# Kernel tuning notes

Measured on AMD Instinct MI355X. Metric: run time of the kernel, lower is better.

## Reference

```python
import jax, jax.numpy as jnp
import numpy as np

N_USERS = 50000
N_ITEMS = 100000
N_ENT = 200000
N_REL_TOTAL = 32  # n_relations * 2
DIM = 64
N_INTENTS = 2
N_LAYERS = 1
B = 4096
E_KG = 2_000_000
E_UI_HALF = 1_000_000  # user->item interactions; symmetrized to 2M directed edges


def setup_inputs() -> dict:
    key = jax.random.key(0)
    ks = jax.random.split(key, 16)
    s = 0.05  # xavier-ish scale
    user_emb = jax.random.normal(ks[0], (N_USERS, DIM), jnp.float32) * s
    entity_emb = jax.random.normal(ks[1], (N_ENT, DIM), jnp.float32) * s
    relation_emb = jax.random.normal(ks[2], (N_REL_TOTAL, DIM), jnp.float32) * s
    intent_weights = jax.random.normal(ks[3], (N_INTENTS, N_REL_TOTAL), jnp.float32) * s
    router_w = jax.random.normal(ks[4], (N_INTENTS, DIM), jnp.float32) * s
    router_b = jnp.zeros((N_INTENTS,), jnp.float32)
    kg_w = jax.random.normal(ks[5], (N_LAYERS, DIM, DIM), jnp.float32) * (1.0 / np.sqrt(DIM))
    item2entity = jax.random.randint(ks[6], (N_ITEMS,), 0, N_ENT)
    kg_src = jax.random.randint(ks[7], (E_KG,), 0, N_ENT)
    kg_dst = jax.random.randint(ks[8], (E_KG,), 0, N_ENT)
    kg_rel = jax.random.randint(ks[9], (E_KG,), 0, N_REL_TOTAL)
    # UI bipartite graph, symmetrically normalized (D^-1/2 A D^-1/2), as in _build_ui_graph
    rng = np.random.default_rng(0)
    uu = rng.integers(0, N_USERS, E_UI_HALF)
    ii = rng.integers(0, N_ITEMS, E_UI_HALF) + N_USERS
    rows = np.concatenate([uu, ii])
    cols = np.concatenate([ii, uu])
    n_nodes = N_USERS + N_ITEMS
    deg = np.bincount(rows, minlength=n_nodes).astype(np.float32)
    dinv = np.where(deg > 0, deg ** -0.5, 0.0).astype(np.float32)
    ui_vals = jnp.asarray(dinv[rows] * dinv[cols])
    ui_row = jnp.asarray(rows.astype(np.int32))
    ui_col = jnpseq = jnp.asarray(cols.astype(np.int32))
    u = jax.random.randint(ks[10], (B,), 0, N_USERS)
    i = jax.random.randint(ks[11], (B,), 0, N_ITEMS)
    neg_i = jax.random.randint(ks[12], (B,), 0, N_ITEMS)
    return dict(u=u, i=i, neg_i=neg_i,
                user_emb=user_emb, entity_emb=entity_emb, relation_emb=relation_emb,
                intent_weights=intent_weights, router_w=router_w, router_b=router_b,
                kg_w=kg_w, ui_vals=ui_vals,
                item2entity=item2entity, kg_src=kg_src, kg_dst=kg_dst, kg_rel=kg_rel,
                ui_row=ui_row, ui_col=ui_col)


def _l2norm(x):
    return x / jnp.maximum(jnp.linalg.norm(x, axis=-1, keepdims=True), 1e-12)


def reference(u, i, neg_i, user_emb, entity_emb, relation_emb, intent_weights,
              router_w, router_b, kg_w, ui_vals, item2entity, kg_src, kg_dst,
              kg_rel, ui_row, ui_col):
    n_ent = entity_emb.shape[0]
    # ---- _propagate_kg (dropout in eval mode = identity) ----
    x = entity_emb
    gate = jax.nn.sigmoid(relation_emb[kg_rel])  # [E, D]
    deg = jax.ops.segment_sum(jnp.ones(kg_dst.shape[0], jnp.float32), kg_dst,
                              num_segments=n_ent)
    deg = jnp.maximum(deg, 1.0)[:, None]
    for l in range(kg_w.shape[0]):
        msg = (x[kg_src] @ kg_w[l].T) * gate           # gather + linear + gate
        agg = jax.ops.segment_sum(msg, kg_dst, num_segments=n_ent)
        x = _l2norm(jax.nn.elu(agg / deg + x))
    item_kg = x[item2entity]                            # [n_items, D]
    # ---- _propagate_ui: sparse normalized adj propagation ----
    all_emb = jnp.concatenate([user_emb, item_kg], 0)
    n_nodes = all_emb.shape[0]
    embs = [all_emb]
    for _ in range(N_LAYERS):
        all_emb = jax.ops.segment_sum(ui_vals[:, None] * all_emb[ui_col], ui_row,
                                      num_segments=n_nodes)
        embs.append(all_emb)
    final = jnp.mean(jnp.stack(embs, 1), 1)
    n_users = user_emb.shape[0]
    u_prop, i_prop = final[:n_users], final[n_users:]
    # ---- intent mixing ----
    intent_dist = jax.nn.softmax(u_prop @ router_w.T + router_b, axis=-1)
    intent_emb = jax.nn.softmax(intent_weights, axis=-1) @ relation_emb
    ue = u_prop + intent_dist @ intent_emb
    ie = i_prop + item_kg
    pos = jnp.sum(ue[u] * ie[i], 1)
    neg = jnp.sum(ue[u] * ie[neg_i], 1)
    return pos, neg
```

## Files before the change

kernel.cpp:

```cpp
#include <hip/hip_runtime.h>
#include <math.h>

#define N_USERS 50000
#define N_ITEMS 100000
#define N_ENT   200000
#define N_NODES (N_USERS + N_ITEMS)
#define N_REL   32
#define DIM     64

#define NB_KG  391
#define NB_UI  586
#define NB_TOT (NB_KG + NB_UI)
#define CAPK   4096
#define CAPU   1536
#define NMMTILE 1563
#define NSCAT  768
#define FUSE_GRID (NSCAT + NMMTILE)
#define NCPY   208

__device__ __forceinline__ unsigned short f2bf(float f) {
    unsigned u = __float_as_uint(f);
    u += 0x7FFFu + ((u >> 16) & 1u);
    return (unsigned short)(u >> 16);
}
__device__ __forceinline__ float bf_lo(unsigned v) { return __uint_as_float(v << 16); }
__device__ __forceinline__ float bf_hi(unsigned v) { return __uint_as_float(v & 0xFFFF0000u); }
__device__ __forceinline__ int getbit(const unsigned* m, int i) {
    return (m[i >> 5] >> (i & 31)) & 1;
}

__global__ __launch_bounds__(256) void build_masks(const int* __restrict__ i2e,
                                                   const int* __restrict__ u,
                                                   const int* __restrict__ ipos,
                                                   const int* __restrict__ ineg,
                                                   const float* __restrict__ rel_emb,
                                                   float2* __restrict__ gateg,
                                                   unsigned* __restrict__ ent_mask,
                                                   unsigned* __restrict__ node_mask,
                                                   int* __restrict__ bcur,
                                                   int B) {
    int t = blockIdx.x * 256 + threadIdx.x;
    int stride = gridDim.x * 256;
    for (int i = threadIdx.x; i < NB_TOT; i += 256)
        bcur[i] = (i < NB_KG) ? i * CAPK : (i - NB_KG) * CAPU;
    if (blockIdx.x == 0) {
        for (int idx = threadIdx.x; idx < N_REL * 32; idx += 256) {
            int rel = idx >> 5, hl2 = idx & 31;
            float g0 = 1.0f / (1.0f + __expf(-rel_emb[rel * 64 + 2 * hl2]));
            float g1 = 1.0f / (1.0f + __expf(-rel_emb[rel * 64 + 2 * hl2 + 1]));
            gateg[idx] = make_float2(g0, g1);
        }
    }
    for (int i = t; i < N_ITEMS; i += stride) {
        int e = i2e[i];
        atomicOr(&ent_mask[e >> 5], 1u << (e & 31));
    }
    for (int i = t; i < 3 * B; i += stride) {
        int r = (i < B) ? u[i]
              : (i < 2 * B) ? N_USERS + ipos[i - B]
                            : N_USERS + ineg[i - 2 * B];
        atomicOr(&node_mask[r >> 5], 1u << (r & 31));
    }
}

__global__ __launch_bounds__(512) void mm_scatter(const float* __restrict__ x,
                                                  const float* __restrict__ w,
                                                  unsigned short* __restrict__ y16,
                                                  int n_ent,
                                                  const int* __restrict__ kg_src,
                                                  const int* __restrict__ kg_dst,
                                                  const int* __restrict__ kg_rel,
                                                  const int* __restrict__ ui_row,
                                                  const int* __restrict__ ui_col,
                                                  const float* __restrict__ ui_vals,
                                                  const unsigned* __restrict__ ent_mask,
                                                  const unsigned* __restrict__ node_mask,
                                                  int* __restrict__ bcur,
                                                  unsigned int* __restrict__ kgrec,
                                                  int* __restrict__ uirec,
                                                  float* __restrict__ uval,
                                                  int e_kg, int e_ui) {
    __shared__ __align__(16) char smem[49152];
    int tid = threadIdx.x;
    int bid = blockIdx.x;

    if (bid < NSCAT) {
        int* h     = (int*)smem;
        int* lbase = h + NB_TOT;
        int n = e_kg + e_ui;
        int nchunks = (n + 4095) >> 12;
        for (int c = bid; c < nchunks; c += NSCAT) {
            int base = c << 12;
            for (int i = tid; i < NB_TOT; i += 512) h[i] = 0;
            __syncthreads();
            unsigned int rec[8];
            float val[8];
            int bk[8];
            #pragma unroll
            for (int j = 0; j < 8; j++) {
                int e = base + j * 512 + tid;
                bk[j] = -1;
                if (e < n) {
                    if (e < e_kg) {
                        int d = kg_dst[e];
                        if (getbit(ent_mask, d)) {
                            bk[j]  = d >> 9;
                            rec[j] = (unsigned int)kg_src[e]
                                     | ((unsigned int)kg_rel[e] << 18)
                                     | ((unsigned int)(d & 511) << 23);
                            atomicAdd(&h[bk[j]], 1);
                        }
                    } else {
                        int i2 = e - e_kg;
                        int r  = ui_row[i2];
                        if (getbit(node_mask, r)) {
                            bk[j]  = NB_KG + (r >> 8);
                            rec[j] = (unsigned int)ui_col[i2]
                                     | ((unsigned int)(r & 255) << 18);
                            val[j] = ui_vals[i2];
                            atomicAdd(&h[bk[j]], 1);
                        }
                    }
                }
            }
            __syncthreads();
            for (int i = tid; i < NB_TOT; i += 512) {
                int cc = h[i];
                lbase[i] = cc ? atomicAdd(&bcur[i], cc) : 0;
            }
            __syncthreads();
            #pragma unroll
            for (int j = 0; j < 8; j++) {
                if (bk[j] >= 0) {
                    int pos = atomicAdd(&lbase[bk[j]], 1);
                    if (bk[j] < NB_KG) {
                        if (pos < (bk[j] + 1) * CAPK) kgrec[pos] = rec[j];
                    } else {
                        int bu = bk[j] - NB_KG;
                        if (pos < (bu + 1) * CAPU) { uirec[pos] = (int)rec[j]; uval[pos] = val[j]; }
                    }
                }
            }
            __syncthreads();
        }
        return;
    }

    int mtile = bid - NSCAT;
    float (*xt)[128] = (float (*)[128])smem;
    float (*wt)[64]  = (float (*)[64])(smem + 32768);
    int base = mtile * 128;

    #pragma unroll
    for (int q = 0; q < 2; q++) {
        int idx = q * 512 + tid;
        int j = idx >> 4, k4 = idx & 15;
        int s0 = (k4 << 2) & 28;
        float4 v = ((const float4*)w)[idx];
        wt[4 * k4 + 0][j ^ s0] = v.x;
        wt[4 * k4 + 1][j ^ s0] = v.y;
        wt[4 * k4 + 2][j ^ s0] = v.z;
        wt[4 * k4 + 3][j ^ s0] = v.w;
    }
    #pragma unroll
    for (int q = 0; q < 4; q++) {
        int idx = q * 512 + tid;
        int r = idx >> 4, k4 = idx & 15;
        int gr = base + r;
        int s0 = (k4 << 2) & 28;
        if (gr < n_ent) {
            float4 v = ((const float4*)x)[(long)gr * 16 + k4];
            xt[4 * k4 + 0][r ^ s0] = v.x;
            xt[4 * k4 + 1][r ^ s0] = v.y;
            xt[4 * k4 + 2][r ^ s0] = v.z;
            xt[4 * k4 + 3][r ^ s0] = v.w;
        }
    }
    __syncthreads();

    int j0 = (tid & 7) * 8;
    int r0 = (tid >> 3) * 2;
    float acc[2][8];
    #pragma unroll
    for (int i = 0; i < 2; i++)
        #pragma unroll
        for (int j = 0; j < 8; j++) acc[i][j] = 0.f;

    #pragma unroll 4
    for (int k = 0; k < 64; k++) {
        int s = k & 28;
        float2 xa = *(const float2*)&xt[k][r0 ^ s];
        float4 wa = *(const float4*)&wt[k][j0 ^ s];
        float4 wb = *(const float4*)&wt[k][(j0 + 4) ^ s];
        float xr[2] = {xa.x, xa.y};
        float wr[8] = {wa.x, wa.y, wa.z, wa.w, wb.x, wb.y, wb.z, wb.w};
        #pragma unroll
        for (int i = 0; i < 2; i++)
            #pragma unroll
            for (int j = 0; j < 8; j++)
                acc[i][j] += xr[i] * wr[j];
    }

    #pragma unroll
    for (int i = 0; i < 2; i++) {
        int gr = base + r0 + i;
        if (gr < n_ent) {
            uint4 o;
            o.x = (unsigned)f2bf(acc[i][0]) | ((unsigned)f2bf(acc[i][1]) << 16);
            o.y = (unsigned)f2bf(acc[i][2]) | ((unsigned)f2bf(acc[i][3]) << 16);
            o.z = (unsigned)f2bf(acc[i][4]) | ((unsigned)f2bf(acc[i][5]) << 16);
            o.w = (unsigned)f2bf(acc[i][6]) | ((unsigned)f2bf(acc[i][7]) << 16);
            *(uint4*)&y16[(long)gr * 64 + j0] = o;
        }
    }
}

__global__ __launch_bounds__(256) void bucket_finalize(const int* __restrict__ bcur,
                                                       unsigned int* __restrict__ kgrec,
                                                       int* __restrict__ uirec,
                                                       float* __restrict__ uval,
                                                       int* __restrict__ beg_kg,
                                                       int* __restrict__ end_kg,
                                                       int* __restrict__ beg_ui,
                                                       int* __restrict__ end_ui,
                                                       const float* __restrict__ user_emb,
                                                       unsigned short* __restrict__ all16) {
    __shared__ unsigned int rec[CAPK];
    __shared__ float fval[CAPU];
    __shared__ int hist[512];
    int tid = threadIdx.x;

    if (blockIdx.x >= NB_TOT) {
        int cid = blockIdx.x - NB_TOT;
        const float4* ue4 = (const float4*)user_emb;
        uint2* a2 = (uint2*)all16;
        int total = N_USERS * 16;
        for (int i = cid * 256 + tid; i < total; i += NCPY * 256) {
            float4 v = ue4[i];
            a2[i] = make_uint2((unsigned)f2bf(v.x) | ((unsigned)f2bf(v.y) << 16),
                               (unsigned)f2bf(v.z) | ((unsigned)f2bf(v.w) << 16));
        }
        return;
    }

    bool iskg = blockIdx.x < NB_KG;
    int  b    = iskg ? blockIdx.x : blockIdx.x - NB_KG;
    int base  = iskg ? b * CAPK : b * CAPU;
    int cap   = iskg ? CAPK : CAPU;
    int ne    = min(bcur[blockIdx.x] - base, cap);
    int key_base = iskg ? (b << 9) : (b << 8);
    int nkeys = iskg ? min(512, N_ENT - key_base) : min(256, N_NODES - key_base);
    int SH = iskg ? 23 : 18;

    for (int i = tid; i < ne; i += 256) {
        if (iskg) rec[i] = kgrec[base + i];
        else { rec[i] = (unsigned int)uirec[base + i]; fval[i] = uval[base + i]; }
    }
    for (int i = tid; i < 512; i += 256) hist[i] = 0;
    __syncthreads();
    for (int i = tid; i < ne; i += 256)
        atomicAdd(&hist[rec[i] >> SH], 1);
    __syncthreads();
    int i0 = tid, i1 = tid + 256;
    int v0 = hist[i0], v1 = hist[i1];
    __syncthreads();
    for (int o = 1; o < 512; o <<= 1) {
        int a0 = (i0 >= o) ? hist[i0 - o] : 0;
        int a1 = (i1 >= o) ? hist[i1 - o] : 0;
        __syncthreads();
        hist[i0] += a0; hist[i1] += a1;
        __syncthreads();
    }
    int e0 = hist[i0] - v0, e1 = hist[i1] - v1;
    __syncthreads();
    hist[i0] = e0; hist[i1] = e1;
    int* begg = iskg ? beg_kg : beg_ui;
    int* endg = iskg ? end_kg : end_ui;
    if (i0 < nkeys) { begg[key_base + i0] = base + e0; endg[key_base + i0] = base + e0 + v0; }
    if (i1 < nkeys) { begg[key_base + i1] = base + e1; endg[key_base + i1] = base + e1 + v1; }
    __syncthreads();
    for (int i = tid; i < ne; i += 256) {
        unsigned int r = rec[i];
        int k = r >> SH;
        int slot = atomicAdd(&hist[k], 1);
        if (iskg) kgrec[base + slot] = r & 0x7FFFFFu;
        else      { uirec[base + slot] = (int)(r & 0x3FFFFu); uval[base + slot] = fval[i]; }
    }
}

__global__ __launch_bounds__(256) void kgagg_build(const int* __restrict__ beg_kg,
                                                   const int* __restrict__ end_kg,
                                                   const unsigned int* __restrict__ packed,
                                                   const unsigned short* __restrict__ y16,
                                                   const float* __restrict__ entity_emb,
                                                   const int* __restrict__ i2e,
                                                   const float4* __restrict__ gate4,
                                                   const unsigned* __restrict__ node_mask,
                                                   float* __restrict__ all_emb,
                                                   unsigned short* __restrict__ all16) {
    int lane = threadIdx.x & 63;
    int half = lane >> 5;
    int hl   = lane & 31;
    int duo  = hl >> 4;
    int ql   = hl & 15;
    long wpair = (long)((blockIdx.x * 256 + threadIdx.x) >> 6);
    int it = (int)(wpair * 2 + half);
    if (it >= N_ITEMS) return;
    int w = N_USERS + it;

    int ent = i2e[it];
    const uint2* y2 = (const uint2*)y16;
    int beg = beg_kg[ent], end = end_kg[ent];
    float a0 = 0.f, a1 = 0.f, a2 = 0.f, a3 = 0.f;
    float b0 = 0.f, b1 = 0.f, b2 = 0.f, b3 = 0.f;
    int p = beg;
    for (; p + 4 <= end; p += 4) {
        unsigned pk0 = packed[p + duo];
        unsigned pk1 = packed[p + 2 + duo];
        uint2 v0 = y2[(long)(pk0 & 0x3FFFF) * 16 + ql];
        uint2 v1 = y2[(long)(pk1 & 0x3FFFF) * 16 + ql];
        float4 g0 = gate4[(pk0 >> 18) * 16 + ql];
        float4 g1 = gate4[(pk1 >> 18) * 16 + ql];
        a0 += bf_lo(v0.x) * g0.x;  a1 += bf_hi(v0.x) * g0.y;
        a2 += bf_lo(v0.y) * g0.z;  a3 += bf_hi(v0.y) * g0.w;
        b0 += bf_lo(v1.x) * g1.x;  b1 += bf_hi(v1.x) * g1.y;
        b2 += bf_lo(v1.y) * g1.z;  b3 += bf_hi(v1.y) * g1.w;
    }
    if (p + duo < end) {
        unsigned pk = packed[p + duo];
        uint2 v = y2[(long)(pk & 0x3FFFF) * 16 + ql];
        float4 g = gate4[(pk >> 18) * 16 + ql];
        a0 += bf_lo(v.x) * g.x;  a1 += bf_hi(v.x) * g.y;
        a2 += bf_lo(v.y) * g.z;  a3 += bf_hi(v.y) * g.w;
    }
    if (p + 2 + duo < end) {
        unsigned pk = packed[p + 2 + duo];
        uint2 v = y2[(long)(pk & 0x3FFFF) * 16 + ql];
        float4 g = gate4[(pk >> 18) * 16 + ql];
        b0 += bf_lo(v.x) * g.x;  b1 += bf_hi(v.x) * g.y;
        b2 += bf_lo(v.y) * g.z;  b3 += bf_hi(v.y) * g.w;
    }
    a0 += b0; a1 += b1; a2 += b2; a3 += b3;
    a0 += __shfl_xor(a0, 16);
    a1 += __shfl_xor(a1, 16);
    a2 += __shfl_xor(a2, 16);
    a3 += __shfl_xor(a3, 16);

    float deg = fmaxf((float)(end - beg), 1.0f);
    float4 xv = ((const float4*)entity_emb)[(long)ent * 16 + ql];
    float v0 = a0 / deg + xv.x;
    float v1 = a1 / deg + xv.y;
    float v2 = a2 / deg + xv.z;
    float v3 = a3 / deg + xv.w;
    v0 = (v0 > 0.0f) ? v0 : (__expf(v0) - 1.0f);
    v1 = (v1 > 0.0f) ? v1 : (__expf(v1) - 1.0f);
    v2 = (v2 > 0.0f) ? v2 : (__expf(v2) - 1.0f);
    v3 = (v3 > 0.0f) ? v3 : (__expf(v3) - 1.0f);
    float ss = v0 * v0 + v1 * v1 + v2 * v2 + v3 * v3;
    ss += __shfl_xor(ss, 1);
    ss += __shfl_xor(ss, 2);
    ss += __shfl_xor(ss, 4);
    ss += __shfl_xor(ss, 8);
    float inv = 1.0f / fmaxf(sqrtf(ss), 1e-12f);
    if (duo == 0) {
        float r0 = v0 * inv, r1 = v1 * inv, r2 = v2 * inv, r3 = v3 * inv;
        if (getbit(node_mask, w))
            ((float4*)all_emb)[(long)w * 16 + ql] = make_float4(r0, r1, r2, r3);
        ((uint2*)all16)[(long)w * 16 + ql] =
            make_uint2((unsigned)f2bf(r0) | ((unsigned)f2bf(r1) << 16),
                       (unsigned)f2bf(r2) | ((unsigned)f2bf(r3) << 16));
    }
}

__global__ __launch_bounds__(256) void ui_aggregate_s(const int* __restrict__ beg_ui,
                                                      const int* __restrict__ end_ui,
                                                      const int* __restrict__ colrec,
                                                      const float* __restrict__ uval,
                                                      const float* __restrict__ all_emb,
                                                      const float* __restrict__ user_emb,
                                                      const unsigned short* __restrict__ all16,
                                                      const int* __restrict__ u,
                                                      const int* __restrict__ ipos,
                                                      const int* __restrict__ ineg,
                                                      float* __restrict__ final_emb, int B) {
    const uint2* a2p = (const uint2*)all16;
    int lane = threadIdx.x & 63;
    int half = lane >> 5;
    int hl   = lane & 31;
    int duo  = hl >> 4;
    int ql   = hl & 15;
    long wpair = (long)((blockIdx.x * 256 + threadIdx.x) >> 6);
    int s = (int)(wpair * 2 + half);
    if (s >= 3 * B) return;
    int r;
    if (s < B)          r = u[s];
    else if (s < 2 * B) r = N_USERS + ipos[s - B];
    else                r = N_USERS + ineg[s - 2 * B];

    int beg = beg_ui[r], end = end_ui[r];
    float a0 = 0.f, a1 = 0.f, a2 = 0.f, a3 = 0.f;
    float b0 = 0.f, b1 = 0.f, b2 = 0.f, b3 = 0.f;
    int p = beg;
    for (; p + 4 <= end; p += 4) {
        int   c0 = colrec[p + duo];
        int   c1 = colrec[p + 2 + duo];
        float d0 = uval[p + duo];
        float d1 = uval[p + 2 + duo];
        uint2 v0 = a2p[(long)c0 * 16 + ql];
        uint2 v1 = a2p[(long)c1 * 16 + ql];
        a0 += d0 * bf_lo(v0.x);  a1 += d0 * bf_hi(v0.x);
        a2 += d0 * bf_lo(v0.y);  a3 += d0 * bf_hi(v0.y);
        b0 += d1 * bf_lo(v1.x);  b1 += d1 * bf_hi(v1.x);
        b2 += d1 * bf_lo(v1.y);  b3 += d1 * bf_hi(v1.y);
    }
    if (p + duo < end) {
        int   c = colrec[p + duo];
        float d = uval[p + duo];
        uint2 v = a2p[(long)c * 16 + ql];
        a0 += d * bf_lo(v.x);  a1 += d * bf_hi(v.x);
        a2 += d * bf_lo(v.y);  a3 += d * bf_hi(v.y);
    }
    if (p + 2 + duo < end) {
        int   c = colrec[p + 2 + duo];
        float d = uval[p + 2 + duo];
        uint2 v = a2p[(long)c * 16 + ql];
        b0 += d * bf_lo(v.x);  b1 += d * bf_hi(v.x);
        b2 += d * bf_lo(v.y);  b3 += d * bf_hi(v.y);
    }
    a0 += b0; a1 += b1; a2 += b2; a3 += b3;
    a0 += __shfl_xor(a0, 16);
    a1 += __shfl_xor(a1, 16);
    a2 += __shfl_xor(a2, 16);
    a3 += __shfl_xor(a3, 16);
    if (duo == 0) {
        float4 ae = (r < N_USERS)
            ? ((const float4*)user_emb)[(long)r * 16 + ql]
            : ((const float4*)all_emb)[(long)r * 16 + ql];
        ((float4*)final_emb)[(long)r * 16 + ql] =
            make_float4(0.5f * (ae.x + a0), 0.5f * (ae.y + a1),
                        0.5f * (ae.z + a2), 0.5f * (ae.w + a3));
    }
}

__global__ void final_kernel(const int* __restrict__ u, const int* __restrict__ ipos,
                             const int* __restrict__ ineg,
                             const float* __restrict__ final_emb,
                             const float* __restrict__ all_emb,
                             const float* __restrict__ rw, const float* __restrict__ rb,
                             const float* __restrict__ iw, const float* __restrict__ rel_emb,
                             float* __restrict__ out, int B) {
    __shared__ float sh_intent[128];
    if (threadIdx.x < 64) {
        int j = threadIdx.x;
        for (int k = 0; k < 2; k++) {
            float m = -1e30f;
            for (int r = 0; r < N_REL; r++) m = fmaxf(m, iw[k * N_REL + r]);
            float Z = 0.f, acc = 0.f;
            for (int r = 0; r < N_REL; r++) {
                float e = __expf(iw[k * N_REL + r] - m);
                Z += e;
                acc += e * rel_emb[r * 64 + j];
            }
            sh_intent[k * 64 + j] = acc / Z;
        }
    }
    __syncthreads();
    int lane = threadIdx.x & 63;
    int wave = (blockIdx.x * blockDim.x + threadIdx.x) >> 6;
    int nw   = (gridDim.x * blockDim.x) >> 6;
    for (int b = wave; b < B; b += nw) {
        int uu = u[b];
        float up = final_emb[(long)uu * 64 + lane];
        float l0 = up * rw[lane];
        float l1 = up * rw[64 + lane];
        #pragma unroll
        for (int o = 32; o; o >>= 1) {
            l0 += __shfl_xor(l0, o);
            l1 += __shfl_xor(l1, o);
        }
        l0 += rb[0]; l1 += rb[1];
        float m  = fmaxf(l0, l1);
        float e0 = __expf(l0 - m), e1 = __expf(l1 - m);
        float inv = 1.0f / (e0 + e1);
        float p0 = e0 * inv, p1 = e1 * inv;
        float ue = up + p0 * sh_intent[lane] + p1 * sh_intent[64 + lane];

        int it = ipos[b];
        long rr = (long)(N_USERS + it) * 64 + lane;
        float ie = final_emb[rr] + all_emb[rr];
        float dp = ue * ie;
        #pragma unroll
        for (int o = 32; o; o >>= 1) dp += __shfl_xor(dp, o);
        if (lane == 0) out[b] = dp;

        it = ineg[b];
        rr = (long)(N_USERS + it) * 64 + lane;
        ie = final_emb[rr] + all_emb[rr];
        dp = ue * ie;
        #pragma unroll
        for (int o = 32; o; o >>= 1) dp += __shfl_xor(dp, o);
        if (lane == 0) out[B + b] = dp;
    }
}

extern "C" void kernel_launch(void* const* d_in, const int* in_sizes, int n_in,
                              void* d_out, int out_size, void* d_ws, size_t ws_size,
                              hipStream_t stream) {
    const int*   u          = (const int*)  d_in[0];
    const int*   ipos       = (const int*)  d_in[1];
    const int*   ineg       = (const int*)  d_in[2];
    const float* user_emb   = (const float*)d_in[3];
    const float* entity_emb = (const float*)d_in[4];
    const float* rel_emb    = (const float*)d_in[5];
    const float* iw         = (const float*)d_in[6];
    const float* rw         = (const float*)d_in[7];
    const float* rb         = (const float*)d_in[8];
    const float* kgw        = (const float*)d_in[9];
    const float* ui_vals    = (const float*)d_in[10];
    const int*   i2e        = (const int*)  d_in[11];
    const int*   kg_src     = (const int*)  d_in[12];
    const int*   kg_dst     = (const int*)  d_in[13];
    const int*   kg_rel     = (const int*)  d_in[14];
    const int*   ui_row     = (const int*)  d_in[15];
    const int*   ui_col     = (const int*)  d_in[16];
    float*       out        = (float*)d_out;

    int B    = in_sizes[0];
    int e_kg = in_sizes[12];
    int e_ui = in_sizes[15];

    char* ws = (char*)d_ws;
    unsigned short* y16       = (unsigned short*)(ws + 0);
    float*          all_emb   = (float*)(ws + 25600000);
    unsigned short* all16     = (unsigned short*)(ws + 64000000);
    float*          final_emb = (float*)(ws + 83200000);
    unsigned int*   kgrec     = (unsigned int*)(ws + 121600000);
    int*            end_kg    = (int*)(ws + 128006144);
    int*            end_ui    = (int*)(ws + 128806144);
    int*            uirec     = (int*)(ws + 129600000);
    float*          uval      = (float*)(ws + 133600000);
    int*            beg_kg    = (int*)(ws + 137600000);
    int*            beg_ui    = (int*)(ws + 138400256);
    unsigned*       ent_mask  = (unsigned*)(ws + 139000512);
    unsigned*       node_mask = (unsigned*)(ws + 139025600);
    int*            bcur      = (int*)(ws + 139608704);
    float2*         gateg     = (float2*)(ws + 139612672);

    hipMemsetAsync(ent_mask, 0, 25088 + 18752, stream);
    build_masks<<<512, 256, 0, stream>>>(i2e, u, ipos, ineg, rel_emb, gateg,
                                         ent_mask, node_mask, bcur, B);
    mm_scatter <<<FUSE_GRID, 512, 0, stream>>>(
        entity_emb, kgw, y16, N_ENT,
        kg_src, kg_dst, kg_rel, ui_row, ui_col, ui_vals,
        ent_mask, node_mask, bcur, kgrec, uirec, uval, e_kg, e_ui);
    bucket_finalize<<<NB_TOT + NCPY, 256, 0, stream>>>(bcur, kgrec, uirec, uval,
                                                       beg_kg, end_kg, beg_ui, end_ui,
                                                       user_emb, all16);
    {
        int nwaves = N_ITEMS / 2;
        int nblk   = (nwaves * 64 + 255) / 256;
        kgagg_build<<<nblk, 256, 0, stream>>>(
            beg_kg, end_kg, kgrec, y16, entity_emb, i2e,
            (const float4*)gateg, node_mask, all_emb, all16);
    }
    {
        int nwaves = (3 * B + 1) / 2;
        int nblk   = (nwaves * 64 + 255) / 256;
        ui_aggregate_s<<<nblk, 256, 0, stream>>>(
            beg_ui, end_ui, uirec, uval, all_emb, user_emb, all16,
            u, ipos, ineg, final_emb, B);
    }
    final_kernel<<<256, 256, 0, stream>>>(u, ipos, ineg, final_emb, all_emb,
                                          rw, rb, iw, rel_emb, out, B);
}
```

Measured before the change: 280.3 us.

## Split bucket finalize; fuse UI finalize and user copy into KG aggregation

The combined bucket_finalize kernel is split. KG bucket sorting stays in its own small kernel, while the UI bucket sort and the user-embedding bf16 copy move into extra blocks of the KG aggregation kernel. The UI work does not depend on the KG sort, so it can overlap with KG aggregation instead of sitting in the earlier launch. The cost is larger shared memory per block in the fused kernel, which can lower occupancy for the aggregation blocks.

```diff
diff --git a/kernel.cpp b/kernel.cpp
--- a/kernel.cpp
+++ b/kernel.cpp
@@ -17,6 +17,7 @@
 #define NSCAT  768
 #define FUSE_GRID (NSCAT + NMMTILE)
 #define NCPY   208
+#define KGOFF  (NB_UI + NCPY)
 
 __device__ __forceinline__ unsigned short f2bf(float f) {
     unsigned u = __float_as_uint(f);
@@ -215,51 +216,24 @@
     }
 }
 
-__global__ __launch_bounds__(256) void bucket_finalize(const int* __restrict__ bcur,
-                                                       unsigned int* __restrict__ kgrec,
-                                                       int* __restrict__ uirec,
-                                                       float* __restrict__ uval,
-                                                       int* __restrict__ beg_kg,
-                                                       int* __restrict__ end_kg,
-                                                       int* __restrict__ beg_ui,
-                                                       int* __restrict__ end_ui,
-                                                       const float* __restrict__ user_emb,
-                                                       unsigned short* __restrict__ all16) {
+__global__ __launch_bounds__(256) void finalize_kg(const int* __restrict__ bcur,
+                                                   unsigned int* __restrict__ kgrec,
+                                                   int* __restrict__ beg_kg,
+                                                   int* __restrict__ end_kg) {
     __shared__ unsigned int rec[CAPK];
-    __shared__ float fval[CAPU];
     __shared__ int hist[512];
+    int b    = blockIdx.x;
+    int base = b * CAPK;
+    int ne   = min(bcur[b] - base, CAPK);
+    int key_base = b << 9;
+    int nkeys = min(512, N_ENT - key_base);
     int tid = threadIdx.x;
 
-    if (blockIdx.x >= NB_TOT) {
-        int cid = blockIdx.x - NB_TOT;
-        const float4* ue4 = (const float4*)user_emb;
-        uint2* a2 = (uint2*)all16;
-        int total = N_USERS * 16;
-        for (int i = cid * 256 + tid; i < total; i += NCPY * 256) {
-            float4 v = ue4[i];
-            a2[i] = make_uint2((unsigned)f2bf(v.x) | ((unsigned)f2bf(v.y) << 16),
-                               (unsigned)f2bf(v.z) | ((unsigned)f2bf(v.w) << 16));
-        }
-        return;
-    }
-
-    bool iskg = blockIdx.x < NB_KG;
-    int  b    = iskg ? blockIdx.x : blockIdx.x - NB_KG;
-    int base  = iskg ? b * CAPK : b * CAPU;
-    int cap   = iskg ? CAPK : CAPU;
-    int ne    = min(bcur[blockIdx.x] - base, cap);
-    int key_base = iskg ? (b << 9) : (b << 8);
-    int nkeys = iskg ? min(512, N_ENT - key_base) : min(256, N_NODES - key_base);
-    int SH = iskg ? 23 : 18;
-
-    for (int i = tid; i < ne; i += 256) {
-        if (iskg) rec[i] = kgrec[base + i];
-        else { rec[i] = (unsigned int)uirec[base + i]; fval[i] = uval[base + i]; }
-    }
+    for (int i = tid; i < ne; i += 256) rec[i] = kgrec[base + i];
     for (int i = tid; i < 512; i += 256) hist[i] = 0;
     __syncthreads();
     for (int i = tid; i < ne; i += 256)
-        atomicAdd(&hist[rec[i] >> SH], 1);
+        atomicAdd(&hist[rec[i] >> 23], 1);
     __syncthreads();
     int i0 = tid, i1 = tid + 256;
     int v0 = hist[i0], v1 = hist[i1];
@@ -274,21 +248,23 @@
     int e0 = hist[i0] - v0, e1 = hist[i1] - v1;
     __syncthreads();
     hist[i0] = e0; hist[i1] = e1;
-    int* begg = iskg ? beg_kg : beg_ui;
-    int* endg = iskg ? end_kg : end_ui;
-    if (i0 < nkeys) { begg[key_base + i0] = base + e0; endg[key_base + i0] = base + e0 + v0; }
-    if (i1 < nkeys) { begg[key_base + i1] = base + e1; endg[key_base + i1] = base + e1 + v1; }
+    if (i0 < nkeys) { beg_kg[key_base + i0] = base + e0; end_kg[key_base + i0] = base + e0 + v0; }
+    if (i1 < nkeys) { beg_kg[key_base + i1] = base + e1; end_kg[key_base + i1] = base + e1 + v1; }
     __syncthreads();
     for (int i = tid; i < ne; i += 256) {
         unsigned int r = rec[i];
-        int k = r >> SH;
-        int slot = atomicAdd(&hist[k], 1);
-        if (iskg) kgrec[base + slot] = r & 0x7FFFFFu;
-        else      { uirec[base + slot] = (int)(r & 0x3FFFFu); uval[base + slot] = fval[i]; }
-    }
-}
-
-__global__ __launch_bounds__(256) void kgagg_build(const int* __restrict__ beg_kg,
+        int slot = atomicAdd(&hist[r >> 23], 1);
+        kgrec[base + slot] = r & 0x7FFFFFu;
+    }
+}
+
+__global__ __launch_bounds__(256) void kgagg_fused(const int* __restrict__ bcur,
+                                                   int* __restrict__ uirec,
+                                                   float* __restrict__ uval,
+                                                   int* __restrict__ beg_ui,
+                                                   int* __restrict__ end_ui,
+                                                   const float* __restrict__ user_emb,
+                                                   const int* __restrict__ beg_kg,
                                                    const int* __restrict__ end_kg,
                                                    const unsigned int* __restrict__ packed,
                                                    const unsigned short* __restrict__ y16,
@@ -298,12 +274,74 @@
                                                    const unsigned* __restrict__ node_mask,
                                                    float* __restrict__ all_emb,
                                                    unsigned short* __restrict__ all16) {
-    int lane = threadIdx.x & 63;
+    __shared__ __align__(16) char smem[14336];
+    int tid = threadIdx.x;
+    int bid = blockIdx.x;
+
+    if (bid < NB_UI) {
+        unsigned int* rec = (unsigned int*)smem;
+        float* fval = (float*)(smem + 6144);
+        int*   hist = (int*)(smem + 12288);
+        int b    = bid;
+        int base = b * CAPU;
+        int ne   = min(bcur[NB_KG + b] - base, CAPU);
+        int key_base = b << 8;
+        int nkeys = min(256, N_NODES - key_base);
+
+        for (int i = tid; i < ne; i += 256) {
+            rec[i] = (unsigned int)uirec[base + i];
+            fval[i] = uval[base + i];
+        }
+        for (int i = tid; i < 512; i += 256) hist[i] = 0;
+        __syncthreads();
+        for (int i = tid; i < ne; i += 256)
+            atomicAdd(&hist[rec[i] >> 18], 1);
+        __syncthreads();
+        int i0 = tid, i1 = tid + 256;
+        int v0 = hist[i0], v1 = hist[i1];
+        __syncthreads();
+        for (int o = 1; o < 512; o <<= 1) {
+            int a0 = (i0 >= o) ? hist[i0 - o] : 0;
+            int a1 = (i1 >= o) ? hist[i1 - o] : 0;
+            __syncthreads();
+            hist[i0] += a0; hist[i1] += a1;
+            __syncthreads();
+        }
+        int e0 = hist[i0] - v0, e1 = hist[i1] - v1;
+        __syncthreads();
+        hist[i0] = e0; hist[i1] = e1;
+        if (i0 < nkeys) { beg_ui[key_base + i0] = base + e0; end_ui[key_base + i0] = base + e0 + v0; }
+        if (i1 < nkeys) { beg_ui[key_base + i1] = base + e1; end_ui[key_base + i1] = base + e1 + v1; }
+        __syncthreads();
+        for (int i = tid; i < ne; i += 256) {
+            unsigned int r = rec[i];
+            int slot = atomicAdd(&hist[r >> 18], 1);
+            uirec[base + slot] = (int)(r & 0x3FFFFu);
+            uval[base + slot] = fval[i];
+        }
+        return;
+    }
+
+    if (bid < KGOFF) {
+        int cid = bid - NB_UI;
+        const float4* ue4 = (const float4*)user_emb;
+        uint2* a2 = (uint2*)all16;
+        int total = N_USERS * 16;
+        for (int i = cid * 256 + tid; i < total; i += NCPY * 256) {
+            float4 v = ue4[i];
+            a2[i] = make_uint2((unsigned)f2bf(v.x) | ((unsigned)f2bf(v.y) << 16),
+                               (unsigned)f2bf(v.z) | ((unsigned)f2bf(v.w) << 16));
+        }
+        return;
+    }
+
+    int kblk = bid - KGOFF;
+    int lane = tid & 63;
     int half = lane >> 5;
     int hl   = lane & 31;
     int duo  = hl >> 4;
     int ql   = hl & 15;
-    long wpair = (long)((blockIdx.x * 256 + threadIdx.x) >> 6);
+    long wpair = (long)((kblk * 256 + tid) >> 6);
     int it = (int)(wpair * 2 + half);
     if (it >= N_ITEMS) return;
     int w = N_USERS + it;
@@ -553,13 +591,12 @@
         entity_emb, kgw, y16, N_ENT,
         kg_src, kg_dst, kg_rel, ui_row, ui_col, ui_vals,
         ent_mask, node_mask, bcur, kgrec, uirec, uval, e_kg, e_ui);
-    bucket_finalize<<<NB_TOT + NCPY, 256, 0, stream>>>(bcur, kgrec, uirec, uval,
-                                                       beg_kg, end_kg, beg_ui, end_ui,
-                                                       user_emb, all16);
+    finalize_kg<<<NB_KG, 256, 0, stream>>>(bcur, kgrec, beg_kg, end_kg);
     {
         int nwaves = N_ITEMS / 2;
-        int nblk   = (nwaves * 64 + 255) / 256;
-        kgagg_build<<<nblk, 256, 0, stream>>>(
+        int nkblk  = (nwaves * 64 + 255) / 256;
+        kgagg_fused<<<KGOFF + nkblk, 256, 0, stream>>>(
+            bcur, uirec, uval, beg_ui, end_ui, user_emb,
             beg_kg, end_kg, kgrec, y16, entity_emb, i2e,
             (const float4*)gateg, node_mask, all_emb, all16);
     }
```

New measurement: 279.0 us. Within noise of the previous version (-0.4%).
